# Optimization experiments

Measured on AMD Instinct MI355X. Metric: run time of the kernel, lower is better.

Reference implementation:

```python
import jax, jax.numpy as jnp
import numpy as np

N_NODES = 100000
N_EDGES = 3200000
N_FEAT = 512
N_GRAPHS = 64
N_EXTRA_LAYERS = 3  # layers 2..4, all 1->1


def setup_inputs() -> dict:
    key = jax.random.key(0)
    ks = jax.random.split(key, 10)
    x = jax.random.normal(ks[0], (N_NODES, N_FEAT), dtype=jnp.float32)
    edge_src = jax.random.randint(ks[1], (N_EDGES,), 0, N_NODES, dtype=jnp.int32)
    edge_dst = jax.random.randint(ks[2], (N_EDGES,), 0, N_NODES, dtype=jnp.int32)
    graph_ids = jnp.sort(jax.random.randint(ks[3], (N_NODES,), 0, N_GRAPHS, dtype=jnp.int32))
    W_neigh0 = jax.random.normal(ks[4], (N_FEAT, 1), dtype=jnp.float32) * 0.05
    W_self0 = jax.random.normal(ks[5], (N_FEAT, 1), dtype=jnp.float32) * 0.05
    b0 = jax.random.normal(ks[6], (1,), dtype=jnp.float32)
    W_neigh_r = jax.random.normal(ks[7], (N_EXTRA_LAYERS, 1, 1), dtype=jnp.float32)
    W_self_r = jax.random.normal(ks[8], (N_EXTRA_LAYERS, 1, 1), dtype=jnp.float32)
    b_r = jax.random.normal(ks[9], (N_EXTRA_LAYERS, 1), dtype=jnp.float32)
    return {"x": x, "edge_src": edge_src, "edge_dst": edge_dst, "graph_ids": graph_ids,
            "W_neigh0": W_neigh0, "W_self0": W_self0, "b0": b0,
            "W_neigh_r": W_neigh_r, "W_self_r": W_self_r, "b_r": b_r}


def _conv_wl(h, edge_src, edge_dst, W_neigh, W_self, b, n_nodes):
    # GraphConv(norm='none'): project first (in >= out here), gather at src, scatter-sum at dst, + bias
    proj = h @ W_neigh                      # [N, out]
    neigh = jax.ops.segment_sum(proj[edge_src], edge_dst, num_segments=n_nodes) + b
    return neigh + h @ W_self               # residual self-loop linear (no bias)


def reference(x, edge_src, edge_dst, graph_ids, W_neigh0, W_self0, b0, W_neigh_r, W_self_r, b_r):
    n = x.shape[0]
    xs = [x]
    h = jax.nn.relu(_conv_wl(x, edge_src, edge_dst, W_neigh0, W_self0, b0, n))
    xs.append(h)
    for i in range(W_neigh_r.shape[0]):
        h = jax.nn.relu(_conv_wl(h, edge_src, edge_dst, W_neigh_r[i], W_self_r[i], b_r[i], n))
        xs.append(h)
    hcat = jnp.concatenate(xs, axis=1)       # [N, F + num_layers] (concat_features=True)
    # dgl.sum_nodes: per-graph sum over the batched graph
    return jax.ops.segment_sum(hcat, graph_ids, num_segments=N_GRAPHS)  # [G, F + L]
```

## Files before the change

kernel.cpp:

```cpp
#include <hip/hip_runtime.h>

#define N_NODES  100000
#define N_EDGES  3200000
#define N_FEAT   512
#define N_GRAPHS 64
#define N_COLS   516
#define NBINS    1563
#define B1       256
#define EPB      (N_EDGES / B1)
#define CHUNK    20
#define NWAVES   (N_NODES / CHUNK)
#define SRC_MASK 0x1FFFF

typedef float f4v __attribute__((ext_vector_type(4)));

__global__ __launch_bounds__(1024) void prep_kernel(
    const int* __restrict__ edst, const int* __restrict__ gid,
    int* __restrict__ histG, int* __restrict__ starts,
    float* __restrict__ outz, int* __restrict__ done)
{
    __shared__ int lh[NBINS];
    const int b = blockIdx.x, tid = threadIdx.x;
    const int gtid = b * 1024 + tid;

    if (gtid == 0) *done = 0;
    if (gtid < N_GRAPHS * N_COLS) outz[gtid] = 0.f;
    if (gtid < N_NODES) {
        const int g = gid[gtid];
        const int gp = gtid ? gid[gtid - 1] : -1;
        for (int q = gp + 1; q <= g; ++q) starts[q] = gtid;
        if (gtid == N_NODES - 1)
            for (int q = g + 1; q <= N_GRAPHS; ++q) starts[q] = N_NODES;
    }
    for (int i = tid; i < NBINS; i += 1024) lh[i] = 0;
    __syncthreads();
    const int e0 = b * EPB;
    for (int e = e0 + tid; e < e0 + EPB; e += 1024)
        atomicAdd(&lh[edst[e] >> 6], 1);
    __syncthreads();
    for (int i = tid; i < NBINS; i += 1024) histG[i * B1 + b] = lh[i];
}

__device__ __forceinline__ void flush_cs(
    int si, int cur_g, const float a[8], int wave, int lane,
    float* __restrict__ pp, int* __restrict__ pt, float* __restrict__ out)
{
    if (si < 2) {
        const int slot = wave * 2 + si;
        if (lane == 0) pt[slot] = cur_g;
        float* d = pp + (size_t)slot * N_FEAT + lane * 8;
        *(float4*)d       = make_float4(a[0], a[1], a[2], a[3]);
        *(float4*)(d + 4) = make_float4(a[4], a[5], a[6], a[7]);
    } else {
        float* o = out + (size_t)cur_g * N_COLS + lane * 8;
        #pragma unroll
        for (int k = 0; k < 8; ++k) atomicAdd(o + k, a[k]);
    }
}

__global__ __launch_bounds__(256) void pass_x_kernel(
    const float* __restrict__ x, const int* __restrict__ gid,
    const float* __restrict__ wn, const float* __restrict__ ws,
    float* __restrict__ p0, float* __restrict__ s0,
    float* __restrict__ out, float* __restrict__ pp, int* __restrict__ pt)
{
    const int wave = (blockIdx.x * blockDim.x + threadIdx.x) >> 6;
    const int lane = threadIdx.x & 63;
    const int start = wave * CHUNK, end = start + CHUNK;

    const float4 wna = *(const float4*)(wn + lane * 8);
    const float4 wnb = *(const float4*)(wn + lane * 8 + 4);
    const float4 wsa = *(const float4*)(ws + lane * 8);
    const float4 wsb = *(const float4*)(ws + lane * 8 + 4);

    float a[8] = {0.f, 0.f, 0.f, 0.f, 0.f, 0.f, 0.f, 0.f};
    int cur_g = gid[start];
    const bool uniform = (gid[end - 1] == cur_g);
    int si = 0;

    for (int n = start; n < end; ++n) {
        if (!uniform) {
            const int g = gid[n];
            if (g != cur_g) {
                flush_cs(si, cur_g, a, wave, lane, pp, pt, out);
                ++si;
                #pragma unroll
                for (int k = 0; k < 8; ++k) a[k] = 0.f;
                cur_g = g;
            }
        }
        const float* row = x + (size_t)n * N_FEAT;
        const f4v xa = __builtin_nontemporal_load((const f4v*)(row + lane * 8));
        const f4v xb = __builtin_nontemporal_load((const f4v*)(row + lane * 8 + 4));

        a[0] += xa.x; a[1] += xa.y; a[2] += xa.z; a[3] += xa.w;
        a[4] += xb.x; a[5] += xb.y; a[6] += xb.z; a[7] += xb.w;

        float dn = xa.x*wna.x + xa.y*wna.y + xa.z*wna.z + xa.w*wna.w
                 + xb.x*wnb.x + xb.y*wnb.y + xb.z*wnb.z + xb.w*wnb.w;
        float dv = xa.x*wsa.x + xa.y*wsa.y + xa.z*wsa.z + xa.w*wsa.w
                 + xb.x*wsb.x + xb.y*wsb.y + xb.z*wsb.z + xb.w*wsb.w;
        #pragma unroll
        for (int off = 32; off > 0; off >>= 1) {
            dn += __shfl_down(dn, off);
            dv += __shfl_down(dv, off);
        }
        if (lane == 0) { p0[n] = dn; s0[n] = dv; }
    }
    flush_cs(si, cur_g, a, wave, lane, pp, pt, out);
    ++si;
    if (lane == 0)
        for (int s2 = si; s2 < 2; ++s2) pt[wave * 2 + s2] = -1;
}

__global__ __launch_bounds__(256) void scan_fused_kernel(
    const int* __restrict__ histG, int* __restrict__ colscanG,
    int* __restrict__ totalG, int* __restrict__ binstart, int* __restrict__ done)
{
    __shared__ int sc[256];
    __shared__ int lastflag;
    const int bin = blockIdx.x, t = threadIdx.x;
    const int v = histG[bin * B1 + t];
    sc[t] = v;
    __syncthreads();
    for (int off = 1; off < 256; off <<= 1) {
        const int a = (t >= off) ? sc[t - off] : 0;
        __syncthreads();
        sc[t] += a;
        __syncthreads();
    }
    colscanG[bin * B1 + t] = sc[t] - v;
    if (t == 255) totalG[bin] = sc[255];

    __threadfence();
    if (t == 0) lastflag = (atomicAdd(done, 1) == NBINS - 1);
    __syncthreads();
    if (!lastflag) return;
    __threadfence();

    const int CH = 7;
    int loc[CH];
    int s = 0;
    for (int i = 0; i < CH; ++i) {
        const int b2 = t * CH + i;
        const int vv = (b2 < NBINS) ? totalG[b2] : 0;
        loc[i] = s; s += vv;
    }
    const int my = s;
    __syncthreads();
    sc[t] = my;
    __syncthreads();
    for (int off = 1; off < 256; off <<= 1) {
        const int a = (t >= off) ? sc[t - off] : 0;
        __syncthreads();
        sc[t] += a;
        __syncthreads();
    }
    const int texcl = sc[t] - my;
    for (int i = 0; i < CH; ++i) {
        const int b2 = t * CH + i;
        if (b2 < NBINS) binstart[b2] = texcl + loc[i];
    }
    if (t == 255) binstart[NBINS] = sc[255];
}

__global__ __launch_bounds__(1024) void reorder_reduce_kernel(
    const int* __restrict__ esrc, const int* __restrict__ edst,
    const int* __restrict__ binstart, const int* __restrict__ colscanG,
    int* __restrict__ sorted,
    const float* __restrict__ pp, const int* __restrict__ pt,
    const int* __restrict__ starts, float* __restrict__ out)
{
    const int b = blockIdx.x, tid = threadIdx.x;
    if (b < B1) {
        __shared__ int offs[NBINS];
        for (int i = tid; i < NBINS; i += 1024)
            offs[i] = binstart[i] + colscanG[i * B1 + b];
        __syncthreads();
        const int e0 = b * EPB;
        for (int e = e0 + tid; e < e0 + EPB; e += 1024) {
            const int s = esrc[e], d = edst[e];
            const int p = atomicAdd(&offs[d >> 6], 1);
            sorted[p] = s | ((d & 63) << 17);
        }
    } else {
        const int g = (b - B1) * 2 + (tid >> 9);
        const int c = tid & 511;
        const int s = starts[g], e = starts[g + 1];
        float acc = 0.f;
        if (e > s) {
            const int w0 = s / CHUNK, w1 = (e - 1) / CHUNK;
            for (int w = w0; w <= w1; ++w) {
                #pragma unroll
                for (int k = 0; k < 2; ++k) {
                    const int slot = w * 2 + k;
                    if (pt[slot] == g) acc += pp[(size_t)slot * N_FEAT + c];
                }
            }
        }
        out[(size_t)g * N_COLS + c] += acc;
    }
}

__global__ __launch_bounds__(256) void binned_scatter_kernel(
    const int* __restrict__ sorted, const int* __restrict__ binstart,
    const float* __restrict__ pin, const float* __restrict__ self_in,
    const float* __restrict__ wself_p, const float* __restrict__ bias_p,
    const float* __restrict__ wnext_p,
    float* __restrict__ h_out, float* __restrict__ p_next,
    const int* __restrict__ gid, float* __restrict__ out, int col)
{
    __shared__ float acc[4][64];
    const int b = blockIdx.x, tid = threadIdx.x;
    ((float*)acc)[tid] = 0.f;
    __syncthreads();

    const int st = binstart[b], en = binstart[b + 1];
    const int w = tid >> 6;
    for (int e = st + tid; e < en; e += 256) {
        const int v = sorted[e];
        atomicAdd(&acc[w][v >> 17], pin[v & SRC_MASK]);
    }
    __syncthreads();

    if (tid < 64) {
        const int n = b * 64 + tid;
        const bool valid = (n < N_NODES);
        float h = 0.f;
        int g = 0;
        if (valid) {
            const float nb = acc[0][tid] + acc[1][tid] + acc[2][tid] + acc[3][tid];
            const float sw = wself_p ? *wself_p : 1.0f;
            const float v = nb + *bias_p + sw * self_in[n];
            h = v > 0.f ? v : 0.f;
            h_out[n] = h;
            if (wnext_p) p_next[n] = h * (*wnext_p);
            g = gid[n];
        }
        const int g0 = __shfl(g, 0);
        if (__all(!valid || g == g0)) {
            float s = h;
            #pragma unroll
            for (int off = 32; off > 0; off >>= 1) s += __shfl_down(s, off);
            if (tid == 0) atomicAdd(&out[(size_t)g0 * N_COLS + col], s);
        } else if (valid) {
            atomicAdd(&out[(size_t)g * N_COLS + col], h);
        }
    }
}

extern "C" void kernel_launch(void* const* d_in, const int* in_sizes, int n_in,
                              void* d_out, int out_size, void* d_ws, size_t ws_size,
                              hipStream_t stream)
{
    (void)in_sizes; (void)n_in; (void)out_size; (void)ws_size;

    const float* x    = (const float*)d_in[0];
    const int*   esrc = (const int*)d_in[1];
    const int*   edst = (const int*)d_in[2];
    const int*   gid  = (const int*)d_in[3];
    const float* Wn0  = (const float*)d_in[4];
    const float* Ws0  = (const float*)d_in[5];
    const float* b0p  = (const float*)d_in[6];
    const float* Wnr  = (const float*)d_in[7];
    const float* Wsr  = (const float*)d_in[8];
    const float* brp  = (const float*)d_in[9];
    float* out = (float*)d_out;

    float* pp    = (float*)d_ws;
    float* bufP  = pp + (size_t)NWAVES * 2 * N_FEAT;
    float* bufP2 = bufP  + N_NODES;
    float* bufS  = bufP2 + N_NODES;
    float* bufH  = bufS  + N_NODES;
    int*   pt       = (int*)(bufH + N_NODES);
    int*   starts   = pt + NWAVES * 2;
    int*   binstart = starts + (N_GRAPHS + 1);
    int*   totalG   = binstart + NBINS + 1;
    int*   done     = totalG + NBINS;
    int*   histG    = done + 1;
    int*   colscanG = histG + (size_t)NBINS * B1;
    int*   sorted   = colscanG + (size_t)NBINS * B1;

    prep_kernel<<<B1, 1024, 0, stream>>>(edst, gid, histG, starts, out, done);
    pass_x_kernel<<<NWAVES / 4, 256, 0, stream>>>(
        x, gid, Wn0, Ws0, bufP, bufS, out, pp, pt);
    scan_fused_kernel<<<NBINS, 256, 0, stream>>>(
        histG, colscanG, totalG, binstart, done);
    reorder_reduce_kernel<<<B1 + N_GRAPHS / 2, 1024, 0, stream>>>(
        esrc, edst, binstart, colscanG, sorted, pp, pt, starts, out);

    binned_scatter_kernel<<<NBINS, 256, 0, stream>>>(
        sorted, binstart, bufP, bufS, nullptr, b0p, Wnr + 0, bufH, bufP2, gid, out, 512);
    binned_scatter_kernel<<<NBINS, 256, 0, stream>>>(
        sorted, binstart, bufP2, bufH, Wsr + 0, brp + 0, Wnr + 1, bufH, bufP, gid, out, 513);
    binned_scatter_kernel<<<NBINS, 256, 0, stream>>>(
        sorted, binstart, bufP, bufH, Wsr + 1, brp + 1, Wnr + 2, bufH, bufP2, gid, out, 514);
    binned_scatter_kernel<<<NBINS, 256, 0, stream>>>(
        sorted, binstart, bufP2, bufH, Wsr + 2, brp + 2, nullptr, bufH, nullptr, gid, out, 515);
}
```

Measured before the change: 614.3 us.

## Fuse edge histogram prep with x pass into one launch

Merges the edge-destination histogram and graph-start prep kernel with the x-streaming projection and per-graph-sum kernel. Block index selects the role, so the latency-bound histogram work runs alongside the bandwidth-bound read of x and one launch boundary goes away. Prep blocks drop from 1024 to 256 threads. The per-wave chunk also grows from 20 to 25 nodes with three partial-sum slots, and the x loads switch from nontemporal to plain loads. One risk: the prep blocks zero the output while x-pass blocks could atomically add into it, which is safe only because the overflow path is not reached with these graph sizes.

```diff
diff --git a/kernel.cpp b/kernel.cpp
--- a/kernel.cpp
+++ b/kernel.cpp
@@ -8,45 +8,18 @@
 #define NBINS    1563
 #define B1       256
 #define EPB      (N_EDGES / B1)
-#define CHUNK    20
+#define CHUNK    25
 #define NWAVES   (N_NODES / CHUNK)
+#define PXB      (NWAVES / 4)
+#define NSLOT    3
 #define SRC_MASK 0x1FFFF
-
-typedef float f4v __attribute__((ext_vector_type(4)));
-
-__global__ __launch_bounds__(1024) void prep_kernel(
-    const int* __restrict__ edst, const int* __restrict__ gid,
-    int* __restrict__ histG, int* __restrict__ starts,
-    float* __restrict__ outz, int* __restrict__ done)
-{
-    __shared__ int lh[NBINS];
-    const int b = blockIdx.x, tid = threadIdx.x;
-    const int gtid = b * 1024 + tid;
-
-    if (gtid == 0) *done = 0;
-    if (gtid < N_GRAPHS * N_COLS) outz[gtid] = 0.f;
-    if (gtid < N_NODES) {
-        const int g = gid[gtid];
-        const int gp = gtid ? gid[gtid - 1] : -1;
-        for (int q = gp + 1; q <= g; ++q) starts[q] = gtid;
-        if (gtid == N_NODES - 1)
-            for (int q = g + 1; q <= N_GRAPHS; ++q) starts[q] = N_NODES;
-    }
-    for (int i = tid; i < NBINS; i += 1024) lh[i] = 0;
-    __syncthreads();
-    const int e0 = b * EPB;
-    for (int e = e0 + tid; e < e0 + EPB; e += 1024)
-        atomicAdd(&lh[edst[e] >> 6], 1);
-    __syncthreads();
-    for (int i = tid; i < NBINS; i += 1024) histG[i * B1 + b] = lh[i];
-}
 
 __device__ __forceinline__ void flush_cs(
     int si, int cur_g, const float a[8], int wave, int lane,
     float* __restrict__ pp, int* __restrict__ pt, float* __restrict__ out)
 {
-    if (si < 2) {
-        const int slot = wave * 2 + si;
+    if (si < NSLOT) {
+        const int slot = wave * NSLOT + si;
         if (lane == 0) pt[slot] = cur_g;
         float* d = pp + (size_t)slot * N_FEAT + lane * 8;
         *(float4*)d       = make_float4(a[0], a[1], a[2], a[3]);
@@ -58,14 +31,40 @@
     }
 }
 
-__global__ __launch_bounds__(256) void pass_x_kernel(
+__global__ __launch_bounds__(256) void prep_passx_kernel(
     const float* __restrict__ x, const int* __restrict__ gid,
+    const int* __restrict__ edst,
     const float* __restrict__ wn, const float* __restrict__ ws,
     float* __restrict__ p0, float* __restrict__ s0,
-    float* __restrict__ out, float* __restrict__ pp, int* __restrict__ pt)
-{
-    const int wave = (blockIdx.x * blockDim.x + threadIdx.x) >> 6;
-    const int lane = threadIdx.x & 63;
+    float* __restrict__ out, float* __restrict__ pp, int* __restrict__ pt,
+    int* __restrict__ histG, int* __restrict__ starts, int* __restrict__ done)
+{
+    __shared__ int lh[NBINS];
+    const int b = blockIdx.x, tid = threadIdx.x;
+
+    if (b < B1) {
+        const int gtid = b * 256 + tid;
+        if (gtid == 0) *done = 0;
+        if (gtid < N_GRAPHS * N_COLS) out[gtid] = 0.f;
+        for (int n = gtid; n < N_NODES; n += B1 * 256) {
+            const int g = gid[n];
+            const int gp = n ? gid[n - 1] : -1;
+            for (int q = gp + 1; q <= g; ++q) starts[q] = n;
+            if (n == N_NODES - 1)
+                for (int q = g + 1; q <= N_GRAPHS; ++q) starts[q] = N_NODES;
+        }
+        for (int i = tid; i < NBINS; i += 256) lh[i] = 0;
+        __syncthreads();
+        const int e0 = b * EPB;
+        for (int e = e0 + tid; e < e0 + EPB; e += 256)
+            atomicAdd(&lh[edst[e] >> 6], 1);
+        __syncthreads();
+        for (int i = tid; i < NBINS; i += 256) histG[i * B1 + b] = lh[i];
+        return;
+    }
+
+    const int wave = (b - B1) * 4 + (tid >> 6);
+    const int lane = tid & 63;
     const int start = wave * CHUNK, end = start + CHUNK;
 
     const float4 wna = *(const float4*)(wn + lane * 8);
@@ -90,8 +89,8 @@
             }
         }
         const float* row = x + (size_t)n * N_FEAT;
-        const f4v xa = __builtin_nontemporal_load((const f4v*)(row + lane * 8));
-        const f4v xb = __builtin_nontemporal_load((const f4v*)(row + lane * 8 + 4));
+        const float4 xa = *(const float4*)(row + lane * 8);
+        const float4 xb = *(const float4*)(row + lane * 8 + 4);
 
         a[0] += xa.x; a[1] += xa.y; a[2] += xa.z; a[3] += xa.w;
         a[4] += xb.x; a[5] += xb.y; a[6] += xb.z; a[7] += xb.w;
@@ -110,7 +109,7 @@
     flush_cs(si, cur_g, a, wave, lane, pp, pt, out);
     ++si;
     if (lane == 0)
-        for (int s2 = si; s2 < 2; ++s2) pt[wave * 2 + s2] = -1;
+        for (int s2 = si; s2 < NSLOT; ++s2) pt[wave * NSLOT + s2] = -1;
 }
 
 __global__ __launch_bounds__(256) void scan_fused_kernel(
@@ -192,8 +191,8 @@
             const int w0 = s / CHUNK, w1 = (e - 1) / CHUNK;
             for (int w = w0; w <= w1; ++w) {
                 #pragma unroll
-                for (int k = 0; k < 2; ++k) {
-                    const int slot = w * 2 + k;
+                for (int k = 0; k < NSLOT; ++k) {
+                    const int slot = w * NSLOT + k;
                     if (pt[slot] == g) acc += pp[(size_t)slot * N_FEAT + c];
                 }
             }
@@ -268,12 +267,12 @@
     float* out = (float*)d_out;
 
     float* pp    = (float*)d_ws;
-    float* bufP  = pp + (size_t)NWAVES * 2 * N_FEAT;
+    float* bufP  = pp + (size_t)NWAVES * NSLOT * N_FEAT;
     float* bufP2 = bufP  + N_NODES;
     float* bufS  = bufP2 + N_NODES;
     float* bufH  = bufS  + N_NODES;
     int*   pt       = (int*)(bufH + N_NODES);
-    int*   starts   = pt + NWAVES * 2;
+    int*   starts   = pt + NWAVES * NSLOT;
     int*   binstart = starts + (N_GRAPHS + 1);
     int*   totalG   = binstart + NBINS + 1;
     int*   done     = totalG + NBINS;
@@ -281,9 +280,8 @@
     int*   colscanG = histG + (size_t)NBINS * B1;
     int*   sorted   = colscanG + (size_t)NBINS * B1;
 
-    prep_kernel<<<B1, 1024, 0, stream>>>(edst, gid, histG, starts, out, done);
-    pass_x_kernel<<<NWAVES / 4, 256, 0, stream>>>(
-        x, gid, Wn0, Ws0, bufP, bufS, out, pp, pt);
+    prep_passx_kernel<<<B1 + PXB, 256, 0, stream>>>(
+        x, gid, edst, Wn0, Ws0, bufP, bufS, out, pp, pt, histG, starts, done);
     scan_fused_kernel<<<NBINS, 256, 0, stream>>>(
         histG, colscanG, totalG, binstart, done);
     reorder_reduce_kernel<<<B1 + N_GRAPHS / 2, 1024, 0, stream>>>(
```

Measured after the change: 632.6 us. +3.0%, slower.
